# Kernel tuning notes

Hardware: AMD Instinct MI355X
Metric: run time of the kernel (lower is better)

## Reference

```python
import jax, jax.numpy as jnp
import numpy as np

B, D, T = 16, 256, 4096
K = 1024
COMMITMENT_COST = 0.25


def setup_inputs() -> dict:
    key = jax.random.key(0)
    k1, k2 = jax.random.split(key)
    z = jax.random.normal(k1, (B, D, T), dtype=jnp.float32)
    # codebook initialized uniform(-1/K, 1/K) as in the torch module
    embeddings = jax.random.uniform(k2, (K, D), dtype=jnp.float32,
                                    minval=-1.0 / K, maxval=1.0 / K)
    return {"z": z, "embeddings": embeddings}


def reference(z, embeddings):
    # z: (B, D, T) -> (B, T, D)
    zt = jnp.transpose(z, (0, 2, 1))
    flat_z = zt.reshape(-1, D)  # (N, D), N = B*T
    # squared L2 distances to every codebook entry: (N, K)
    distances = (jnp.sum(flat_z * flat_z, axis=1, keepdims=True)
                 + jnp.sum(embeddings * embeddings, axis=1)
                 - 2.0 * flat_z @ embeddings.T)
    indices = jnp.argmin(distances, axis=1)  # (N,)
    # gather replaces the one-hot @ embeddings matmul (same result)
    quantized = embeddings[indices].reshape(B, T, D)
    # commitment loss (quantized detached)
    e_latent_loss = jnp.mean((jax.lax.stop_gradient(quantized) - zt) ** 2)
    loss = COMMITMENT_COST * e_latent_loss
    # straight-through estimator
    quantized_ste = zt + jax.lax.stop_gradient(quantized - zt)
    # perplexity from mean of one-hot encodings = normalized code histogram
    counts = jnp.zeros((K,), dtype=jnp.float32).at[indices].add(1.0)
    avg_probs = counts / flat_z.shape[0]
    perplexity = jnp.exp(-jnp.sum(avg_probs * jnp.log(avg_probs + 1e-10)))
    out = jnp.transpose(quantized_ste, (0, 2, 1))  # (B, D, T)
    return out, indices.reshape(B, T), loss, perplexity
```

## Files before the change

### kernel.cpp

```cpp
#include <hip/hip_runtime.h>
#include <hip/hip_bf16.h>

#define BB 16
#define DDIM 256
#define TLEN 4096
#define KCODES 1024
#define NQ (BB*TLEN)
#define QB 64
#define MAXC 32

#define FLT_MAX_C 3.402823466e+38f

using short8 = __attribute__((ext_vector_type(8))) short;
using f32x4  = __attribute__((ext_vector_type(4))) float;

__device__ __forceinline__ unsigned short f2bf(float x) {
  unsigned u = __float_as_uint(x);
  unsigned r = (u + 0x7fffu + ((u >> 16) & 1u)) >> 16;
  return (unsigned short)r;
}
__device__ __forceinline__ float bf2f(unsigned short h) {
  return __uint_as_float(((unsigned)h) << 16);
}

__device__ __forceinline__ float np_sumsq_256(const float* p, int stride) {
  float th[2];
#pragma unroll
  for (int h = 0; h < 2; ++h) {
    const float* q = p + (size_t)h * 128 * (size_t)stride;
    float r[8];
#pragma unroll
    for (int j = 0; j < 8; ++j) {
      float v = q[(size_t)j * (size_t)stride];
      r[j] = __fmul_rn(v, v);
    }
    for (int i = 8; i < 128; i += 8) {
#pragma unroll
      for (int j = 0; j < 8; ++j) {
        float v = q[(size_t)(i + j) * (size_t)stride];
        r[j] = __fadd_rn(r[j], __fmul_rn(v, v));
      }
    }
    th[h] = __fadd_rn(__fadd_rn(__fadd_rn(r[0], r[1]), __fadd_rn(r[2], r[3])),
                      __fadd_rn(__fadd_rn(r[4], r[5]), __fadd_rn(r[6], r[7])));
  }
  return __fadd_rn(th[0], th[1]);
}

__global__ void k_prep(const float* __restrict__ emb, float* __restrict__ embT,
                       float* __restrict__ e2, short* __restrict__ ebh,
                       unsigned* __restrict__ maxe) {
  const int k = blockIdx.x;
  const int d = threadIdx.x;
  __shared__ float row[DDIM];
  float v = emb[(size_t)k * DDIM + d];
  row[d] = v;
  embT[(size_t)d * KCODES + k] = v;
  ebh[(size_t)k * DDIM + d] = (short)f2bf(v);
  float a = fabsf(v);
#pragma unroll
  for (int m = 1; m < 64; m <<= 1) a = fmaxf(a, __shfl_xor(a, m, 64));
  if ((threadIdx.x & 63) == 0) atomicMax(maxe, __float_as_uint(a));
  __syncthreads();
  if (d == 0) e2[k] = np_sumsq_256(row, 1);
}

__global__ __launch_bounds__(512, 1)
void k_mdist(const float* __restrict__ z, const float* __restrict__ emb,
             const short* __restrict__ ebh, const float* __restrict__ e2,
             const unsigned* __restrict__ maxeU, int* __restrict__ idx,
             int* __restrict__ hist, double* __restrict__ lossp) {
  extern __shared__ __align__(16) char sbuf[];
  float*  zf  = (float*)sbuf;
  short8* abh = (short8*)(sbuf + 65536);
  float* z2s  = (float*)(sbuf + 65536);
  float* sabs = (float*)(sbuf + 65536 + 256);
  float* sm   = (float*)(sbuf + 65536 + 512);
  float* qmin = (float*)(sbuf + 65536 + 2560);
  int*   cnt  = (int*)(sbuf + 65536 + 2816);
  int*   ovf  = (int*)(sbuf + 65536 + 3072);
  int*   cand = (int*)(sbuf + 65536 + 3328);
  float* bd   = (float*)(sbuf + 65536 + 11520);
  int*   bk   = (int*)(sbuf + 65536 + 13568);

  const int tid = threadIdx.x;
  const int lane = tid & 63;
  const int w = tid >> 6;
  const int g = lane >> 4;
  const int c = lane & 15;
  const int n0 = blockIdx.x * QB;
  const int kb = w * 128;
  const float* zp = z + (size_t)(n0 >> 12) * DDIM * TLEN + (n0 & (TLEN - 1));

#pragma unroll
  for (int i = 0; i < 8; ++i) {
    int s4 = i * 512 + tid;
    int d = s4 >> 4, q4 = (s4 & 15) * 4;
    *(float4*)&zf[d * QB + q4] = *(const float4*)(zp + (size_t)d * TLEN + q4);
  }
  __syncthreads();

#pragma unroll
  for (int i = 0; i < 4; ++i) {
    int s = i * 512 + tid;
    int ks = s >> 8, mt = (s >> 6) & 3, ln = s & 63;
    int q = mt * 16 + (ln & 15);
    int d0 = ks * 32 + (ln >> 4) * 8;
    short8 h;
#pragma unroll
    for (int j = 0; j < 8; ++j) h[j] = (short)f2bf(zf[(d0 + j) * QB + q]);
    abh[s] = h;
  }
  __syncthreads();

  f32x4 acc[4][8];
#pragma unroll
  for (int mt = 0; mt < 4; ++mt)
#pragma unroll
    for (int nt = 0; nt < 8; ++nt) {
      f32x4 zz = {0.f, 0.f, 0.f, 0.f};
      acc[mt][nt] = zz;
    }

  const short* ebp = ebh + (size_t)(kb + c) * DDIM + g * 8;
  short8 pb0 = *(const short8*)(ebp);
  short8 pb1 = *(const short8*)(ebp + 16 * DDIM);

  for (int ks = 0; ks < 8; ++ks) {
    short8 ah[4];
#pragma unroll
    for (int mt = 0; mt < 4; ++mt) ah[mt] = abh[ks * 256 + mt * 64 + lane];
#pragma unroll
    for (int nt = 0; nt < 8; ++nt) {
      short8 bh = (nt & 1) ? pb1 : pb0;
      int m = (ks * 8 + nt + 2) & 63;
      size_t off = (size_t)(m & 7) * (16 * DDIM) + (size_t)(m >> 3) * 32;
      short8 nv = *(const short8*)(ebp + off);
      if (nt & 1) pb1 = nv; else pb0 = nv;
#pragma unroll
      for (int mt = 0; mt < 4; ++mt)
        acc[mt][nt] =
            __builtin_amdgcn_mfma_f32_16x16x32_bf16(ah[mt], bh, acc[mt][nt], 0, 0, 0);
    }
  }
  __syncthreads();

  if (tid < QB) {
    z2s[tid] = np_sumsq_256(&zf[tid], QB);
    float sa = 0.f;
    for (int d = 0; d < DDIM; ++d) sa += fabsf(zf[d * QB + tid]);
    sabs[tid] = sa;
    cnt[tid] = 0;
    ovf[tid] = 0;
  }

  const float maxe = __uint_as_float(*maxeU);

  float e2c[8];
#pragma unroll
  for (int nt = 0; nt < 8; ++nt) e2c[nt] = e2[kb + nt * 16 + c];

  float smin[4][4];
#pragma unroll
  for (int mt = 0; mt < 4; ++mt)
#pragma unroll
    for (int r = 0; r < 4; ++r) {
      float m = FLT_MAX_C;
#pragma unroll
      for (int nt = 0; nt < 8; ++nt)
        m = fminf(m, e2c[nt] - 2.0f * acc[mt][nt][r]);
      smin[mt][r] = m;
    }
#pragma unroll
  for (int mt = 0; mt < 4; ++mt)
#pragma unroll
    for (int r = 0; r < 4; ++r) {
#pragma unroll
      for (int m = 1; m < 16; m <<= 1)
        smin[mt][r] = fminf(smin[mt][r], __shfl_xor(smin[mt][r], m, 64));
    }
  if (c == 0) {
#pragma unroll
    for (int mt = 0; mt < 4; ++mt)
#pragma unroll
      for (int r = 0; r < 4; ++r)
        sm[w * QB + mt * 16 + g * 4 + r] = smin[mt][r];
  }
  __syncthreads();
  if (tid < QB) {
    float m = sm[tid];
#pragma unroll
    for (int wv = 1; wv < 8; ++wv) m = fminf(m, sm[wv * QB + tid]);
    qmin[tid] = m;
  }
  __syncthreads();

#pragma unroll
  for (int mt = 0; mt < 4; ++mt)
#pragma unroll
    for (int r = 0; r < 4; ++r) {
      const int ql = mt * 16 + g * 4 + r;
      const float lim = qmin[ql] + (maxe * sabs[ql]) * 0.009f + 2e-4f;
#pragma unroll
      for (int nt = 0; nt < 8; ++nt) {
        float s = e2c[nt] - 2.0f * acc[mt][nt][r];
        if (s <= lim) {
          int p = atomicAdd(&cnt[ql], 1);
          if (p < MAXC) cand[ql * MAXC + p] = kb + nt * 16 + c;
          else ovf[ql] = 1;
        }
      }
    }
  __syncthreads();

  {
    const int q = tid & 63;
    const int slot = tid >> 6;
    const float z2q = z2s[q];
    float bestd = FLT_MAX_C;
    int besti = (1 << 30);
    const bool all = (ovf[q] != 0) || (cnt[q] > MAXC);
    const int count = all ? KCODES : cnt[q];
    for (int ci = slot; ci < count; ci += 8) {
      const int k = all ? ci : cand[q * MAXC + ci];
      const float4* ek = (const float4*)(emb + (size_t)k * DDIM);
      float a0 = 0.f;
      for (int dd = 0; dd < 64; ++dd) {
        float4 e4 = ek[dd];
        a0 = __fmaf_rn(zf[(dd * 4 + 0) * QB + q], e4.x, a0);
        a0 = __fmaf_rn(zf[(dd * 4 + 1) * QB + q], e4.y, a0);
        a0 = __fmaf_rn(zf[(dd * 4 + 2) * QB + q], e4.z, a0);
        a0 = __fmaf_rn(zf[(dd * 4 + 3) * QB + q], e4.w, a0);
      }
      float dist = __fsub_rn(__fadd_rn(z2q, e2[k]), __fmul_rn(2.0f, a0));
      if (dist < bestd || (dist == bestd && k < besti)) { bestd = dist; besti = k; }
    }
    bd[q * 8 + slot] = bestd;
    bk[q * 8 + slot] = besti;
  }
  __syncthreads();

  if (tid < QB) {
    float B = bd[tid * 8 + 0];
    int K = bk[tid * 8 + 0];
#pragma unroll
    for (int s = 1; s < 8; ++s) {
      float d2 = bd[tid * 8 + s];
      int k2 = bk[tid * 8 + s];
      if (d2 < B || (d2 == B && k2 < K)) { B = d2; K = k2; }
    }
    idx[n0 + tid] = K;
    atomicAdd(&hist[K], 1);
    double ls = (double)B;
#pragma unroll
    for (int m = 1; m < 64; m <<= 1) ls += __shfl_xor(ls, m, 64);
    if (tid == 0) lossp[blockIdx.x] = ls;
  }
}

__global__ void k_idxout(const int* __restrict__ idx,
                         float* __restrict__ oidx) {
  int n = blockIdx.x * 256 + threadIdx.x;
  oidx[n] = (float)(idx[n] & (KCODES - 1));
}

__global__ void k_gather(const float* __restrict__ embT,
                         const int* __restrict__ idx,
                         float* __restrict__ out) {
  __shared__ float er[KCODES];
  const int blk = blockIdx.x;
  const int bq = blk >> 8;
  const int d = blk & 255;
  const int tid = threadIdx.x;
  *((float4*)&er[tid * 4]) =
      *((const float4*)(embT + (size_t)d * KCODES + tid * 4));
  __syncthreads();
  const int* ip = idx + (size_t)bq * TLEN;
  float* op = out + (size_t)blk * TLEN;
#pragma unroll
  for (int c = 0; c < 16; ++c) {
    int t = c * 256 + tid;
    int kk = ip[t] & (KCODES - 1);
    op[t] = er[kk];
  }
}

__global__ void k_final(const int* __restrict__ hist,
                        const double* __restrict__ lossp,
                        float* __restrict__ out2) {
  const int tid = threadIdx.x;
  double ls = 0.0;
  for (int i = 0; i < 4; ++i) ls += lossp[tid * 4 + i];
  float es = 0.f;
  for (int i = tid; i < KCODES; i += 256) {
    float p = (float)hist[i] / 65536.0f;
    es += p * logf(p + 1e-10f);
  }
#pragma unroll
  for (int m = 1; m < 64; m <<= 1) {
    ls += __shfl_xor(ls, m, 64);
    es += __shfl_xor(es, m, 64);
  }
  __shared__ double lw[4];
  __shared__ float ew[4];
  if ((tid & 63) == 0) { lw[tid >> 6] = ls; ew[tid >> 6] = es; }
  __syncthreads();
  if (tid == 0) {
    double lt = lw[0] + lw[1] + lw[2] + lw[3];
    float et = ew[0] + ew[1] + ew[2] + ew[3];
    float loss = 0.25f * (float)(lt / (double)((long long)NQ * DDIM));
    float perp = expf(-et);
    out2[0] = loss;
    out2[1] = perp;
  }
}

extern "C" void kernel_launch(void* const* d_in, const int* in_sizes, int n_in,
                              void* d_out, int out_size, void* d_ws, size_t ws_size,
                              hipStream_t stream) {
  const float* z = (const float*)d_in[0];
  const float* emb = (const float*)d_in[1];
  float* out = (float*)d_out;

  char* ws = (char*)d_ws;
  float* embT = (float*)(ws);
  float* e2 = (float*)(ws + 1048576);
  int* idx = (int*)(ws + 1052672);
  int* hist = (int*)(ws + 1314816);
  unsigned* maxe = (unsigned*)(ws + 1318912);
  double* lossp = (double*)(ws + 1318920);
  short* ebh = (short*)(ws + 1327120);

  float* oidx = out + ((size_t)out_size - 2 - NQ);
  float* out2 = out + ((size_t)out_size - 2);

  (void)hipFuncSetAttribute((const void*)k_mdist,
                            hipFuncAttributeMaxDynamicSharedMemorySize,
                            98304);

  hipMemsetAsync(hist, 0, KCODES * sizeof(int) + sizeof(unsigned), stream);

  k_prep<<<KCODES, 256, 0, stream>>>(emb, embT, e2, ebh, maxe);
  k_mdist<<<NQ / QB, 512, 98304, stream>>>(z, emb, ebh, e2, maxe, idx, hist,
                                           lossp);
  k_idxout<<<NQ / 256, 256, 0, stream>>>(idx, oidx);
  k_gather<<<BB * DDIM, 256, 0, stream>>>(embT, idx, out);
  k_final<<<1, 256, 0, stream>>>(hist, lossp, out2);
}
```

Measured before the change: 230.6 us.

## Restructure distance kernel for 1024 threads, smaller LDS, fused index output

The main distance kernel now runs 1024-thread blocks. Each wave covers half the queries and one 128-code slice, which halves the MFMA accumulators per wave. The z tile is staged in two halves into a 32 KB static LDS buffer, so LDS use drops and more blocks can be resident, and all eight B fragments are prefetched per k-step. The exact rescoring pass now reads z straight from global memory instead of LDS, using 16 slots per query. The separate index-to-float kernel is folded into the distance kernel, and the gather kernel is vectorised with int4/float4. The risk is that strided global reads of z in the rescoring loop are uncoalesced and may cost more than the occupancy gain.

```diff
diff --git a/kernel.cpp b/kernel.cpp
--- a/kernel.cpp
+++ b/kernel.cpp
@@ -23,28 +23,26 @@
   return __uint_as_float(((unsigned)h) << 16);
 }
 
-__device__ __forceinline__ float np_sumsq_256(const float* p, int stride) {
-  float th[2];
-#pragma unroll
-  for (int h = 0; h < 2; ++h) {
-    const float* q = p + (size_t)h * 128 * (size_t)stride;
-    float r[8];
+__device__ __forceinline__ float np_sumsq_128(const float* q, int stride) {
+  float r[8];
+#pragma unroll
+  for (int j = 0; j < 8; ++j) {
+    float v = q[(size_t)j * (size_t)stride];
+    r[j] = __fmul_rn(v, v);
+  }
+  for (int i = 8; i < 128; i += 8) {
 #pragma unroll
     for (int j = 0; j < 8; ++j) {
-      float v = q[(size_t)j * (size_t)stride];
-      r[j] = __fmul_rn(v, v);
-    }
-    for (int i = 8; i < 128; i += 8) {
-#pragma unroll
-      for (int j = 0; j < 8; ++j) {
-        float v = q[(size_t)(i + j) * (size_t)stride];
-        r[j] = __fadd_rn(r[j], __fmul_rn(v, v));
-      }
-    }
-    th[h] = __fadd_rn(__fadd_rn(__fadd_rn(r[0], r[1]), __fadd_rn(r[2], r[3])),
-                      __fadd_rn(__fadd_rn(r[4], r[5]), __fadd_rn(r[6], r[7])));
-  }
-  return __fadd_rn(th[0], th[1]);
+      float v = q[(size_t)(i + j) * (size_t)stride];
+      r[j] = __fadd_rn(r[j], __fmul_rn(v, v));
+    }
+  }
+  return __fadd_rn(__fadd_rn(__fadd_rn(r[0], r[1]), __fadd_rn(r[2], r[3])),
+                   __fadd_rn(__fadd_rn(r[4], r[5]), __fadd_rn(r[6], r[7])));
+}
+__device__ __forceinline__ float np_sumsq_256s(const float* p, int stride) {
+  return __fadd_rn(np_sumsq_128(p, stride),
+                   np_sumsq_128(p + (size_t)128 * stride, stride));
 }
 
 __global__ void k_prep(const float* __restrict__ emb, float* __restrict__ embT,
@@ -62,60 +60,76 @@
   for (int m = 1; m < 64; m <<= 1) a = fmaxf(a, __shfl_xor(a, m, 64));
   if ((threadIdx.x & 63) == 0) atomicMax(maxe, __float_as_uint(a));
   __syncthreads();
-  if (d == 0) e2[k] = np_sumsq_256(row, 1);
-}
-
-__global__ __launch_bounds__(512, 1)
+  if (d == 0) e2[k] = np_sumsq_256s(row, 1);
+}
+
+__global__ __launch_bounds__(1024, 4)
 void k_mdist(const float* __restrict__ z, const float* __restrict__ emb,
              const short* __restrict__ ebh, const float* __restrict__ e2,
              const unsigned* __restrict__ maxeU, int* __restrict__ idx,
-             int* __restrict__ hist, double* __restrict__ lossp) {
-  extern __shared__ __align__(16) char sbuf[];
-  float*  zf  = (float*)sbuf;
-  short8* abh = (short8*)(sbuf + 65536);
-  float* z2s  = (float*)(sbuf + 65536);
-  float* sabs = (float*)(sbuf + 65536 + 256);
-  float* sm   = (float*)(sbuf + 65536 + 512);
-  float* qmin = (float*)(sbuf + 65536 + 2560);
-  int*   cnt  = (int*)(sbuf + 65536 + 2816);
-  int*   ovf  = (int*)(sbuf + 65536 + 3072);
-  int*   cand = (int*)(sbuf + 65536 + 3328);
-  float* bd   = (float*)(sbuf + 65536 + 11520);
-  int*   bk   = (int*)(sbuf + 65536 + 13568);
+             float* __restrict__ oidx, int* __restrict__ hist,
+             double* __restrict__ lossp) {
+  __shared__ __align__(16) char zbuf[32768];
+  __shared__ __align__(16) short8 abh[2048];
+  __shared__ float z2s[QB];
+  __shared__ float sabs[QB];
+  float* zf   = (float*)zbuf;
+  float* sm   = (float*)zbuf;
+  float* qmin = (float*)(zbuf + 2048);
+  int*   cnt  = (int*)(zbuf + 2304);
+  int*   ovf  = (int*)(zbuf + 2560);
+  int*   cand = (int*)(zbuf + 2816);
+  float* bd   = (float*)(zbuf + 11008);
+  int*   bk   = (int*)(zbuf + 15104);
 
   const int tid = threadIdx.x;
   const int lane = tid & 63;
   const int w = tid >> 6;
   const int g = lane >> 4;
   const int c = lane & 15;
+  const int qh = w >> 3;
+  const int kb = (w & 7) * 128;
   const int n0 = blockIdx.x * QB;
-  const int kb = w * 128;
   const float* zp = z + (size_t)(n0 >> 12) * DDIM * TLEN + (n0 & (TLEN - 1));
 
-#pragma unroll
-  for (int i = 0; i < 8; ++i) {
-    int s4 = i * 512 + tid;
-    int d = s4 >> 4, q4 = (s4 & 15) * 4;
-    *(float4*)&zf[d * QB + q4] = *(const float4*)(zp + (size_t)d * TLEN + q4);
-  }
-  __syncthreads();
-
-#pragma unroll
-  for (int i = 0; i < 4; ++i) {
-    int s = i * 512 + tid;
-    int ks = s >> 8, mt = (s >> 6) & 3, ln = s & 63;
-    int q = mt * 16 + (ln & 15);
-    int d0 = ks * 32 + (ln >> 4) * 8;
-    short8 h;
-#pragma unroll
-    for (int j = 0; j < 8; ++j) h[j] = (short)f2bf(zf[(d0 + j) * QB + q]);
-    abh[s] = h;
-  }
-  __syncthreads();
-
-  f32x4 acc[4][8];
-#pragma unroll
-  for (int mt = 0; mt < 4; ++mt)
+  float th0 = 0.f, sa0 = 0.f;
+
+#pragma unroll
+  for (int h = 0; h < 2; ++h) {
+#pragma unroll
+    for (int i = 0; i < 2; ++i) {
+      int s4 = i * 1024 + tid;
+      int dl = s4 >> 4, q4 = (s4 & 15) * 4;
+      *(float4*)&zf[dl * QB + q4] =
+          *(const float4*)(zp + (size_t)(h * 128 + dl) * TLEN + q4);
+    }
+    __syncthreads();
+    {
+      int s = h * 1024 + tid;
+      int mt = (s >> 6) & 3, ln = s & 63;
+      int q = mt * 16 + (ln & 15);
+      int d0l = ((s >> 8) & 3) * 32 + (ln >> 4) * 8;
+      short8 hh;
+#pragma unroll
+      for (int j = 0; j < 8; ++j) hh[j] = (short)f2bf(zf[(d0l + j) * QB + q]);
+      abh[s] = hh;
+    }
+    if (tid < QB) {
+      float th = np_sumsq_128(&zf[tid], QB);
+      float sa = 0.f;
+      for (int d = 0; d < 128; ++d) sa += fabsf(zf[d * QB + tid]);
+      if (h == 0) { th0 = th; sa0 = sa; }
+      else {
+        z2s[tid] = __fadd_rn(th0, th);
+        sabs[tid] = sa0 + sa;
+      }
+    }
+    __syncthreads();
+  }
+
+  f32x4 acc[2][8];
+#pragma unroll
+  for (int mt = 0; mt < 2; ++mt)
 #pragma unroll
     for (int nt = 0; nt < 8; ++nt) {
       f32x4 zz = {0.f, 0.f, 0.f, 0.f};
@@ -123,83 +137,65 @@
     }
 
   const short* ebp = ebh + (size_t)(kb + c) * DDIM + g * 8;
-  short8 pb0 = *(const short8*)(ebp);
-  short8 pb1 = *(const short8*)(ebp + 16 * DDIM);
+  short8 bbuf[8];
+#pragma unroll
+  for (int nt = 0; nt < 8; ++nt)
+    bbuf[nt] = *(const short8*)(ebp + nt * (16 * DDIM));
 
   for (int ks = 0; ks < 8; ++ks) {
-    short8 ah[4];
-#pragma unroll
-    for (int mt = 0; mt < 4; ++mt) ah[mt] = abh[ks * 256 + mt * 64 + lane];
+    short8 ah0 = abh[ks * 256 + (qh * 2 + 0) * 64 + lane];
+    short8 ah1 = abh[ks * 256 + (qh * 2 + 1) * 64 + lane];
+    const int ksn = (ks + 1) & 7;
 #pragma unroll
     for (int nt = 0; nt < 8; ++nt) {
-      short8 bh = (nt & 1) ? pb1 : pb0;
-      int m = (ks * 8 + nt + 2) & 63;
-      size_t off = (size_t)(m & 7) * (16 * DDIM) + (size_t)(m >> 3) * 32;
-      short8 nv = *(const short8*)(ebp + off);
-      if (nt & 1) pb1 = nv; else pb0 = nv;
-#pragma unroll
-      for (int mt = 0; mt < 4; ++mt)
-        acc[mt][nt] =
-            __builtin_amdgcn_mfma_f32_16x16x32_bf16(ah[mt], bh, acc[mt][nt], 0, 0, 0);
-    }
-  }
-  __syncthreads();
-
-  if (tid < QB) {
-    z2s[tid] = np_sumsq_256(&zf[tid], QB);
-    float sa = 0.f;
-    for (int d = 0; d < DDIM; ++d) sa += fabsf(zf[d * QB + tid]);
-    sabs[tid] = sa;
-    cnt[tid] = 0;
-    ovf[tid] = 0;
+      short8 b = bbuf[nt];
+      bbuf[nt] = *(const short8*)(ebp + nt * (16 * DDIM) + ksn * 32);
+      acc[0][nt] = __builtin_amdgcn_mfma_f32_16x16x32_bf16(ah0, b, acc[0][nt], 0, 0, 0);
+      acc[1][nt] = __builtin_amdgcn_mfma_f32_16x16x32_bf16(ah1, b, acc[1][nt], 0, 0, 0);
+    }
   }
 
   const float maxe = __uint_as_float(*maxeU);
-
   float e2c[8];
 #pragma unroll
   for (int nt = 0; nt < 8; ++nt) e2c[nt] = e2[kb + nt * 16 + c];
 
-  float smin[4][4];
-#pragma unroll
-  for (int mt = 0; mt < 4; ++mt)
+  float smin[2][4];
+#pragma unroll
+  for (int mt = 0; mt < 2; ++mt)
 #pragma unroll
     for (int r = 0; r < 4; ++r) {
       float m = FLT_MAX_C;
 #pragma unroll
       for (int nt = 0; nt < 8; ++nt)
         m = fminf(m, e2c[nt] - 2.0f * acc[mt][nt][r]);
+#pragma unroll
+      for (int s = 1; s < 16; s <<= 1) m = fminf(m, __shfl_xor(m, s, 64));
       smin[mt][r] = m;
     }
-#pragma unroll
-  for (int mt = 0; mt < 4; ++mt)
+  if (c == 0) {
+#pragma unroll
+    for (int mt = 0; mt < 2; ++mt)
+#pragma unroll
+      for (int r = 0; r < 4; ++r)
+        sm[w * 32 + mt * 16 + g * 4 + r] = smin[mt][r];
+  }
+  if (tid < QB) { cnt[tid] = 0; ovf[tid] = 0; }
+  __syncthreads();
+  if (tid < QB) {
+    const int qq = tid >> 5, j = tid & 31;
+    float m = sm[(qq * 8) * 32 + j];
+#pragma unroll
+    for (int kg = 1; kg < 8; ++kg) m = fminf(m, sm[(qq * 8 + kg) * 32 + j]);
+    qmin[tid] = m;
+  }
+  __syncthreads();
+
+#pragma unroll
+  for (int mt = 0; mt < 2; ++mt)
 #pragma unroll
     for (int r = 0; r < 4; ++r) {
-#pragma unroll
-      for (int m = 1; m < 16; m <<= 1)
-        smin[mt][r] = fminf(smin[mt][r], __shfl_xor(smin[mt][r], m, 64));
-    }
-  if (c == 0) {
-#pragma unroll
-    for (int mt = 0; mt < 4; ++mt)
-#pragma unroll
-      for (int r = 0; r < 4; ++r)
-        sm[w * QB + mt * 16 + g * 4 + r] = smin[mt][r];
-  }
-  __syncthreads();
-  if (tid < QB) {
-    float m = sm[tid];
-#pragma unroll
-    for (int wv = 1; wv < 8; ++wv) m = fminf(m, sm[wv * QB + tid]);
-    qmin[tid] = m;
-  }
-  __syncthreads();
-
-#pragma unroll
-  for (int mt = 0; mt < 4; ++mt)
-#pragma unroll
-    for (int r = 0; r < 4; ++r) {
-      const int ql = mt * 16 + g * 4 + r;
+      const int ql = qh * 32 + mt * 16 + g * 4 + r;
       const float lim = qmin[ql] + (maxe * sabs[ql]) * 0.009f + 2e-4f;
 #pragma unroll
       for (int nt = 0; nt < 8; ++nt) {
@@ -217,51 +213,43 @@
     const int q = tid & 63;
     const int slot = tid >> 6;
     const float z2q = z2s[q];
+    const float* zq = zp + q;
     float bestd = FLT_MAX_C;
     int besti = (1 << 30);
     const bool all = (ovf[q] != 0) || (cnt[q] > MAXC);
     const int count = all ? KCODES : cnt[q];
-    for (int ci = slot; ci < count; ci += 8) {
+    for (int ci = slot; ci < count; ci += 16) {
       const int k = all ? ci : cand[q * MAXC + ci];
-      const float4* ek = (const float4*)(emb + (size_t)k * DDIM);
+      const float* ek = emb + (size_t)k * DDIM;
       float a0 = 0.f;
-      for (int dd = 0; dd < 64; ++dd) {
-        float4 e4 = ek[dd];
-        a0 = __fmaf_rn(zf[(dd * 4 + 0) * QB + q], e4.x, a0);
-        a0 = __fmaf_rn(zf[(dd * 4 + 1) * QB + q], e4.y, a0);
-        a0 = __fmaf_rn(zf[(dd * 4 + 2) * QB + q], e4.z, a0);
-        a0 = __fmaf_rn(zf[(dd * 4 + 3) * QB + q], e4.w, a0);
-      }
+      for (int d = 0; d < DDIM; ++d)
+        a0 = __fmaf_rn(zq[(size_t)d * TLEN], ek[d], a0);
       float dist = __fsub_rn(__fadd_rn(z2q, e2[k]), __fmul_rn(2.0f, a0));
       if (dist < bestd || (dist == bestd && k < besti)) { bestd = dist; besti = k; }
     }
-    bd[q * 8 + slot] = bestd;
-    bk[q * 8 + slot] = besti;
+    bd[q * 16 + slot] = bestd;
+    bk[q * 16 + slot] = besti;
   }
   __syncthreads();
 
   if (tid < QB) {
-    float B = bd[tid * 8 + 0];
-    int K = bk[tid * 8 + 0];
-#pragma unroll
-    for (int s = 1; s < 8; ++s) {
-      float d2 = bd[tid * 8 + s];
-      int k2 = bk[tid * 8 + s];
+    float B = bd[tid * 16 + 0];
+    int K = bk[tid * 16 + 0];
+#pragma unroll
+    for (int s = 1; s < 16; ++s) {
+      float d2 = bd[tid * 16 + s];
+      int k2 = bk[tid * 16 + s];
       if (d2 < B || (d2 == B && k2 < K)) { B = d2; K = k2; }
     }
+    K &= (KCODES - 1);
     idx[n0 + tid] = K;
+    oidx[n0 + tid] = (float)K;
     atomicAdd(&hist[K], 1);
     double ls = (double)B;
 #pragma unroll
     for (int m = 1; m < 64; m <<= 1) ls += __shfl_xor(ls, m, 64);
     if (tid == 0) lossp[blockIdx.x] = ls;
   }
-}
-
-__global__ void k_idxout(const int* __restrict__ idx,
-                         float* __restrict__ oidx) {
-  int n = blockIdx.x * 256 + threadIdx.x;
-  oidx[n] = (float)(idx[n] & (KCODES - 1));
 }
 
 __global__ void k_gather(const float* __restrict__ embT,
@@ -278,10 +266,15 @@
   const int* ip = idx + (size_t)bq * TLEN;
   float* op = out + (size_t)blk * TLEN;
 #pragma unroll
-  for (int c = 0; c < 16; ++c) {
-    int t = c * 256 + tid;
-    int kk = ip[t] & (KCODES - 1);
-    op[t] = er[kk];
+  for (int cch = 0; cch < 4; ++cch) {
+    int t0 = cch * 1024 + tid * 4;
+    int4 ii = *(const int4*)&ip[t0];
+    float4 v;
+    v.x = er[ii.x & (KCODES - 1)];
+    v.y = er[ii.y & (KCODES - 1)];
+    v.z = er[ii.z & (KCODES - 1)];
+    v.w = er[ii.w & (KCODES - 1)];
+    *(float4*)&op[t0] = v;
   }
 }
 
@@ -334,16 +327,11 @@
   float* oidx = out + ((size_t)out_size - 2 - NQ);
   float* out2 = out + ((size_t)out_size - 2);
 
-  (void)hipFuncSetAttribute((const void*)k_mdist,
-                            hipFuncAttributeMaxDynamicSharedMemorySize,
-                            98304);
-
   hipMemsetAsync(hist, 0, KCODES * sizeof(int) + sizeof(unsigned), stream);
 
   k_prep<<<KCODES, 256, 0, stream>>>(emb, embT, e2, ebh, maxe);
-  k_mdist<<<NQ / QB, 512, 98304, stream>>>(z, emb, ebh, e2, maxe, idx, hist,
-                                           lossp);
-  k_idxout<<<NQ / 256, 256, 0, stream>>>(idx, oidx);
+  k_mdist<<<NQ / QB, 1024, 0, stream>>>(z, emb, ebh, e2, maxe, idx, oidx,
+                                        hist, lossp);
   k_gather<<<BB * DDIM, 256, 0, stream>>>(embT, idx, out);
   k_final<<<1, 256, 0, stream>>>(hist, lossp, out2);
 }
```

New measurement: 296.8 us. 28.7% more time.
